# Kernel tuning notes

Measured on AMD Instinct MI355X. Metric: run time of the kernel, lower is better.

## Reference

```python
import jax, jax.numpy as jnp
import numpy as np

N = 100000
E = 1600000
D = 128
NUM_LAYERS = 3
NUM_QUANT = 3   # residual quantizer stages
K = 16          # codebook_size
COMMIT_W = 0.25


def setup_inputs() -> dict:
    key = jax.random.key(0)
    ks = jax.random.split(key, 6)
    x = jax.random.normal(ks[0], (N, D), dtype=jnp.float32)
    w_in = jax.random.normal(ks[1], (D, D), dtype=jnp.float32) / np.sqrt(D)
    b_in = jax.random.normal(ks[2], (D,), dtype=jnp.float32) * 0.01
    codebooks = jax.random.normal(ks[3], (NUM_LAYERS, NUM_QUANT, K, D), dtype=jnp.float32)
    edge_row = jax.random.randint(ks[4], (E,), 0, N, dtype=jnp.int32)
    edge_col = jax.random.randint(ks[5], (E,), 0, N, dtype=jnp.int32)
    return {"x": x, "w_in": w_in, "b_in": b_in, "codebooks": codebooks,
            "edge_row": edge_row, "edge_col": edge_col}


def _l2norm(v, eps=1e-12):
    return v / (jnp.linalg.norm(v, axis=-1, keepdims=True) + eps)


def _puregcn_conv(x, edge_row, edge_col):
    # norm = rsqrt(1 + deg); x = norm*x; x = spmm_add(adj, x) + x; x = norm*x
    n = x.shape[0]
    deg = jax.ops.segment_sum(jnp.ones_like(edge_row, dtype=x.dtype), edge_row, num_segments=n)
    norm = jax.lax.rsqrt(1.0 + deg)[:, None]
    h = norm * x
    agg = jax.ops.segment_sum(h[edge_col], edge_row, num_segments=n)  # [N, D]
    return norm * (agg + h)


def _residual_vq(x, cbs):
    # cbs: [NUM_QUANT, K, D]; cosine-sim lookup, EMA codebook (no grad to codebook)
    residual = x
    ids = []
    loss = jnp.float32(0.0)
    for q in range(NUM_QUANT):
        cb = _l2norm(cbs[q])                      # [K, D]
        sim = _l2norm(residual) @ cb.T            # [N, K]
        idx = jnp.argmax(sim, axis=-1)            # [N]
        qv = jax.lax.stop_gradient(cb[idx])       # [N, D]
        loss = loss + COMMIT_W * jnp.mean((residual - qv) ** 2)
        residual = residual - qv
        ids.append(idx.astype(jnp.int32))
    return jnp.stack(ids, axis=1), loss           # [N, NUM_QUANT], scalar


def reference(x, w_in, b_in, codebooks, edge_row, edge_col):
    # xemb: Linear (pure conv path); dropouts identity in eval
    h = x @ w_in + b_in
    id_list = []
    total_commit_loss = jnp.float32(0.0)
    for i in range(NUM_LAYERS):
        x1 = _puregcn_conv(h, edge_row, edge_col)   # lins[i] is Identity/Dropout(eval)
        ids, closs = _residual_vq(x1, codebooks[i])
        id_list.append(ids)
        total_commit_loss = total_commit_loss + closs
        h = x1 + h  # res=True, same width
    id_concat = jnp.concatenate(id_list, axis=1)    # [N, NUM_LAYERS*NUM_QUANT]
    return h, total_commit_loss, id_concat
```

## Files before the change

kernel.cpp:

```cpp
#include <hip/hip_runtime.h>

#define NN 100000
#define EE 1600000
#define DD 128
#define NL 3
#define NQ 3
#define KK 16
#define ROWS_PER_FBLOCK 64
#define FUSED_BLOCKS ((NN + ROWS_PER_FBLOCK - 1) / ROWS_PER_FBLOCK)
#define LPART_COUNT (NL * FUSED_BLOCKS)
#define EPT 8
#define EPB (256 * EPT)
#define MAXDEG 64

#define ISTRIDE 260
#define QSTRIDE (8 * ISTRIDE)
#define LAYER_CBN (NQ * QSTRIDE)
#define RSTRIDE 36
#define RBUF 144

static constexpr size_t OFF_AGG   = 0;
static constexpr size_t OFF_CSRF  = 0;
static constexpr size_t OFF_CURP  = 25600000;
static constexpr size_t OFF_CSR   = 51200000;
static constexpr size_t OFF_CBN   = 57600000;
static constexpr size_t OFF_NORM  = 57904128;
static constexpr size_t OFF_RS    = 59104128;
static constexpr size_t OFF_BSUM  = 59504640;
static constexpr size_t OFF_LPART = 59505152;
static constexpr size_t WS_NEEDED = 59805152;

__global__ __launch_bounds__(256) void k_fill_fixed(const int* __restrict__ erow,
                                                    const int* __restrict__ ecol,
                                                    int* __restrict__ cursorp,
                                                    int* __restrict__ csrf) {
    int base = blockIdx.x * EPB + threadIdx.x;
    int r[EPT], c[EPT], p[EPT];
#pragma unroll
    for (int u = 0; u < EPT; ++u) {
        int e = base + u * 256;
        r[u] = (e < EE) ? erow[e] : -1;
        c[u] = (e < EE) ? ecol[e] : 0;
    }
#pragma unroll
    for (int u = 0; u < EPT; ++u)
        if (r[u] >= 0) p[u] = atomicAdd(&cursorp[r[u] << 4], 1);
#pragma unroll
    for (int u = 0; u < EPT; ++u)
        if (r[u] >= 0 && p[u] < MAXDEG) csrf[r[u] * MAXDEG + p[u]] = c[u];
}

__global__ __launch_bounds__(1024) void k_scan1(const int* __restrict__ cursorp,
                                                int* __restrict__ rs,
                                                int* __restrict__ bsum) {
    __shared__ int s[1024];
    int tid = threadIdx.x;
    int idx = blockIdx.x * 1024 + tid;
    int v = (idx < NN) ? cursorp[idx << 4] : 0;
    s[tid] = v;
    __syncthreads();
    for (int o = 1; o < 1024; o <<= 1) {
        int t2 = s[tid];
        if (tid >= o) t2 += s[tid - o];
        __syncthreads();
        s[tid] = t2;
        __syncthreads();
    }
    if (idx < NN) rs[idx] = s[tid] - v;
    if (tid == 1023) bsum[blockIdx.x] = s[1023];
}

__global__ __launch_bounds__(128) void k_scan2(int* __restrict__ bsum, int nb) {
    __shared__ int s[128];
    int tid = threadIdx.x;
    int v = (tid < nb) ? bsum[tid] : 0;
    s[tid] = v;
    __syncthreads();
    for (int o = 1; o < 128; o <<= 1) {
        int t2 = s[tid];
        if (tid >= o) t2 += s[tid - o];
        __syncthreads();
        s[tid] = t2;
        __syncthreads();
    }
    if (tid < nb) bsum[tid] = s[tid] - v;
}

__global__ __launch_bounds__(1024) void k_scan3(const int* __restrict__ cursorp,
                                                int* __restrict__ rs,
                                                const int* __restrict__ bsum,
                                                float* __restrict__ normf) {
    int idx = blockIdx.x * 1024 + threadIdx.x;
    if (idx < NN) {
        rs[idx] += bsum[blockIdx.x];
        normf[idx] = rsqrtf(1.0f + (float)cursorp[idx << 4]);
    }
    if (idx == 0) rs[NN] = EE;
}

__global__ __launch_bounds__(256) void k_sortcompact(const int* __restrict__ cursorp,
                                                     const int* __restrict__ rs,
                                                     const int* __restrict__ csrf,
                                                     int* __restrict__ csr) {
    int wid = (blockIdx.x * 256 + threadIdx.x) >> 6;
    int l = threadIdx.x & 63;
    if (wid >= NN) return;
    int deg = cursorp[wid << 4];
    if (deg > MAXDEG) deg = MAXDEG;
    if (deg <= 0) return;
    int v = (l < deg) ? csrf[wid * MAXDEG + l] : 0x7fffffff;
    int rank = 0;
#pragma unroll 8
    for (int m = 0; m < 64; ++m) {
        int vm = __shfl(v, m);
        bool less = (vm < v) || (vm == v && m < l);
        rank += (m < deg && less) ? 1 : 0;
    }
    if (l < deg) csr[rs[wid] + rank] = v;
}

__global__ __launch_bounds__(128) void k_cbnorm(const float* __restrict__ cb,
                                                float* __restrict__ cbn) {
    __shared__ float s[128];
    int row = blockIdx.x;
    int tid = threadIdx.x;
    float v = cb[row * DD + tid];
    s[tid] = v * v;
    __syncthreads();
    for (int o = 64; o > 0; o >>= 1) {
        if (tid < o) s[tid] += s[tid + o];
        __syncthreads();
    }
    float inv = 1.0f / (sqrtf(s[0]) + 1e-12f);
    int lq = row >> 4;
    int k  = row & 15;
    int sq = tid >> 5, ii = (tid >> 2) & 7, d = tid & 3;
    cbn[(size_t)lq * QSTRIDE + ii * ISTRIDE + k * 16 + sq * 4 + d] = v * inv;
}

__global__ __launch_bounds__(256) void k_gemm(const float* __restrict__ x,
                                              const float* __restrict__ w,
                                              const float* __restrict__ bias,
                                              float* __restrict__ h) {
    __shared__ float wls[64][DD];
    __shared__ float xs[32][DD];
    int tid = threadIdx.x;
    int rbase = blockIdx.x * 32;
    int cg = tid & 31;
    int rg = tid >> 5;

#pragma unroll
    for (int p = 0; p < 4; ++p) {
        int i = p * 256 + tid;
        int r = i >> 5, c = (i & 31) * 4;
        *(float4*)&xs[r][c] = *(const float4*)&x[(size_t)(rbase + r) * DD + c];
    }

    float4 acc[4];
#pragma unroll
    for (int i = 0; i < 4; ++i) acc[i] = make_float4(0.f, 0.f, 0.f, 0.f);

    for (int chunk = 0; chunk < 2; ++chunk) {
        __syncthreads();
#pragma unroll
        for (int p = 0; p < 8; ++p) {
            int i = p * 256 + tid;
            int kr = i >> 5, c = (i & 31) * 4;
            *(float4*)&wls[kr][c] = *(const float4*)&w[(size_t)(chunk * 64 + kr) * DD + c];
        }
        __syncthreads();
#pragma unroll 4
        for (int kk = 0; kk < 64; ++kk) {
            float4 wv = *(const float4*)&wls[kk][cg * 4];
            int k = chunk * 64 + kk;
#pragma unroll
            for (int i = 0; i < 4; ++i) {
                float xv = xs[rg * 4 + i][k];
                acc[i].x += xv * wv.x; acc[i].y += xv * wv.y;
                acc[i].z += xv * wv.z; acc[i].w += xv * wv.w;
            }
        }
    }

    float4 bv = *(const float4*)&bias[cg * 4];
#pragma unroll
    for (int i = 0; i < 4; ++i) {
        float4 o;
        o.x = acc[i].x + bv.x; o.y = acc[i].y + bv.y;
        o.z = acc[i].z + bv.z; o.w = acc[i].w + bv.w;
        *(float4*)&h[(size_t)(rbase + rg * 4 + i) * DD + cg * 4] = o;
    }
}

__global__ __launch_bounds__(256) void k_spmm(const float* __restrict__ h,
                                              const float* __restrict__ normf,
                                              const int* __restrict__ rs,
                                              const int* __restrict__ csr,
                                              float* __restrict__ agg) {
    int lane = threadIdx.x & 31;
    int slot = threadIdx.x >> 5;
    int r = blockIdx.x * 8 + slot;
    int s0 = rs[r], e0 = rs[r + 1];
    int off = lane << 2;

    float ax = 0.f, ay = 0.f, az = 0.f, aw = 0.f;
    int j = s0;
    for (; j + 16 <= e0; j += 16) {
        int c[16]; float n[16]; float4 v[16];
#pragma unroll
        for (int u = 0; u < 16; ++u) c[u] = csr[j + u];
#pragma unroll
        for (int u = 0; u < 16; ++u) n[u] = normf[c[u]];
#pragma unroll
        for (int u = 0; u < 16; ++u) v[u] = *(const float4*)&h[(size_t)c[u] * DD + off];
#pragma unroll
        for (int u = 0; u < 16; ++u) {
            ax += n[u] * v[u].x; ay += n[u] * v[u].y;
            az += n[u] * v[u].z; aw += n[u] * v[u].w;
        }
    }
    for (; j + 8 <= e0; j += 8) {
        int c[8]; float n[8]; float4 v[8];
#pragma unroll
        for (int u = 0; u < 8; ++u) c[u] = csr[j + u];
#pragma unroll
        for (int u = 0; u < 8; ++u) n[u] = normf[c[u]];
#pragma unroll
        for (int u = 0; u < 8; ++u) v[u] = *(const float4*)&h[(size_t)c[u] * DD + off];
#pragma unroll
        for (int u = 0; u < 8; ++u) {
            ax += n[u] * v[u].x; ay += n[u] * v[u].y;
            az += n[u] * v[u].z; aw += n[u] * v[u].w;
        }
    }
    for (; j + 4 <= e0; j += 4) {
        int c[4]; float n[4]; float4 v[4];
#pragma unroll
        for (int u = 0; u < 4; ++u) c[u] = csr[j + u];
#pragma unroll
        for (int u = 0; u < 4; ++u) n[u] = normf[c[u]];
#pragma unroll
        for (int u = 0; u < 4; ++u) v[u] = *(const float4*)&h[(size_t)c[u] * DD + off];
#pragma unroll
        for (int u = 0; u < 4; ++u) {
            ax += n[u] * v[u].x; ay += n[u] * v[u].y;
            az += n[u] * v[u].z; aw += n[u] * v[u].w;
        }
    }
    for (; j < e0; ++j) {
        int c = csr[j];
        float ns = normf[c];
        float4 v = *(const float4*)&h[(size_t)c * DD + off];
        ax += ns * v.x;
        ay += ns * v.y;
        az += ns * v.z;
        aw += ns * v.w;
    }
    float4 o = {ax, ay, az, aw};
    *(float4*)&agg[(size_t)r * DD + off] = o;
}

__global__ __launch_bounds__(512) void k_fused(const float* __restrict__ agg,
                                               float* __restrict__ h,
                                               const float* __restrict__ normf,
                                               const float* __restrict__ cbn_layer,
                                               float* __restrict__ idsf,
                                               float* __restrict__ lpart,
                                               int layer) {
    __shared__ float cb_s[LAYER_CBN];
    __shared__ float resid_s[8][RBUF];
    __shared__ float wsum[8];
    int tid = threadIdx.x;

    {
        const float4* src = (const float4*)cbn_layer;
        float4* dst = (float4*)cb_s;
        for (int t = tid; t < LAYER_CBN / 4; t += 512) dst[t] = src[t];
    }
    __syncthreads();

    int w = tid >> 6;
    int l = tid & 63;
    int rwrd = (l >> 4) * RSTRIDE + ((2 * l) & 31);
    int sq = l & 3;
    int cb2 = ((l >> 1) & 7) * ISTRIDE + (l >> 4) * 4 + 2 * (l & 1);
    float lsum = 0.f;

    for (int it = 0; it < ROWS_PER_FBLOCK / 8; ++it) {
        int r = blockIdx.x * ROWS_PER_FBLOCK + it * 8 + w;
        if (r < NN) {
            float nr = normf[r];
            float2 hv = *(const float2*)&h[(size_t)r * DD + 2 * l];
            float2 av = *(const float2*)&agg[(size_t)r * DD + 2 * l];
            float x0 = nr * (av.x + nr * hv.x);
            float x1 = nr * (av.y + nr * hv.y);
            float r0 = x0, r1 = x1;

            for (int q = 0; q < NQ; ++q) {
                *(float2*)&resid_s[w][rwrd] = make_float2(r0, r1);

                const float* cbq = &cb_s[q * QSTRIDE];
                const float* rsd = resid_s[w];
                float pd = 0.f;
#pragma unroll
                for (int i = 0; i < 8; ++i) {
                    float4 cv = *(const float4*)&cbq[i * ISTRIDE + l * 4];
                    float4 rv = *(const float4*)&rsd[sq * RSTRIDE + i * 4];
                    pd += cv.x * rv.x + cv.y * rv.y + cv.z * rv.z + cv.w * rv.w;
                }
                pd += __shfl_xor(pd, 1);
                pd += __shfl_xor(pd, 2);

                float best = pd;
                int bk = l >> 2;
                for (int m = 4; m < 64; m <<= 1) {
                    float ov = __shfl_xor(best, m);
                    int oi = __shfl_xor(bk, m);
                    if (ov > best || (ov == best && oi < bk)) { best = ov; bk = oi; }
                }

                float2 cv2 = *(const float2*)&cb_s[q * QSTRIDE + bk * 16 + cb2];
                r0 -= cv2.x;
                r1 -= cv2.y;
                lsum += r0 * r0 + r1 * r1;

                if (l == 0) idsf[(size_t)r * (NL * NQ) + layer * NQ + q] = (float)bk;
            }

            *(float2*)&h[(size_t)r * DD + 2 * l] = make_float2(x0 + hv.x, x1 + hv.y);
        }
    }

#pragma unroll
    for (int m = 1; m < 64; m <<= 1) lsum += __shfl_xor(lsum, m);
    if (l == 0) wsum[w] = lsum;
    __syncthreads();
    if (tid == 0) {
        float tot = 0.f;
#pragma unroll
        for (int i = 0; i < 8; ++i) tot += wsum[i];
        lpart[layer * FUSED_BLOCKS + blockIdx.x] = tot * (0.25f / (float)(NN * DD));
    }
}

__global__ __launch_bounds__(256) void k_loss_reduce(const float* __restrict__ part,
                                                     float* __restrict__ out_loss) {
    __shared__ float s[256];
    float a = 0.f;
    for (int i = threadIdx.x; i < LPART_COUNT; i += 256) a += part[i];
    s[threadIdx.x] = a;
    __syncthreads();
    for (int o = 128; o > 0; o >>= 1) {
        if (threadIdx.x < o) s[threadIdx.x] += s[threadIdx.x + o];
        __syncthreads();
    }
    if (threadIdx.x == 0) out_loss[0] = s[0];
}

extern "C" void kernel_launch(void* const* d_in, const int* in_sizes, int n_in,
                              void* d_out, int out_size, void* d_ws, size_t ws_size,
                              hipStream_t stream) {
    if (ws_size < WS_NEEDED) return;

    const float* x    = (const float*)d_in[0];
    const float* w_in = (const float*)d_in[1];
    const float* b_in = (const float*)d_in[2];
    const float* cbs  = (const float*)d_in[3];
    const int*   erow = (const int*)d_in[4];
    const int*   ecol = (const int*)d_in[5];

    float* out  = (float*)d_out;
    float* hbuf = out;
    float* loss = out + (size_t)NN * DD;
    float* idsf = out + (size_t)NN * DD + 1;

    char* ws = (char*)d_ws;
    float* agg     = (float*)(ws + OFF_AGG);
    int*   csrf    = (int*)(ws + OFF_CSRF);
    int*   cursorp = (int*)(ws + OFF_CURP);
    int*   csr     = (int*)(ws + OFF_CSR);
    float* cbn     = (float*)(ws + OFF_CBN);
    float* normf   = (float*)(ws + OFF_NORM);
    int*   rs      = (int*)(ws + OFF_RS);
    int*   bsum    = (int*)(ws + OFF_BSUM);
    float* lpart   = (float*)(ws + OFF_LPART);

    hipMemsetAsync(ws + OFF_CURP, 0, 6400000, stream);

    const int NB_B  = (EE + EPB - 1) / EPB;
    const int NB_SC = (NN + 1023) / 1024;
    const int NB_W  = (NN + 3) / 4;

    k_fill_fixed<<<NB_B, 256, 0, stream>>>(erow, ecol, cursorp, csrf);
    k_scan1<<<NB_SC, 1024, 0, stream>>>(cursorp, rs, bsum);
    k_scan2<<<1, 128, 0, stream>>>(bsum, NB_SC);
    k_scan3<<<NB_SC, 1024, 0, stream>>>(cursorp, rs, bsum, normf);
    k_sortcompact<<<NB_W, 256, 0, stream>>>(cursorp, rs, csrf, csr);

    k_cbnorm<<<NL * NQ * KK, 128, 0, stream>>>(cbs, cbn);
    k_gemm<<<NN / 32, 256, 0, stream>>>(x, w_in, b_in, hbuf);

    for (int layer = 0; layer < NL; ++layer) {
        k_spmm<<<NN / 8, 256, 0, stream>>>(hbuf, normf, rs, csr, agg);
        k_fused<<<FUSED_BLOCKS, 512, 0, stream>>>(agg, hbuf, normf,
                                                  cbn + (size_t)layer * LAYER_CBN,
                                                  idsf, lpart, layer);
    }

    k_loss_reduce<<<1, 256, 0, stream>>>(lpart, loss);
}
```

Measured before the change: 852.2 us.

## Fuse SpMM gather into per-layer VQ kernel with ping-pong h buffers

Removes the separate SpMM kernel and its agg buffer by doing the neighbor gather-aggregate inside the fused VQ kernel, one 64-lane wave per row using float2 per lane. Layers ping-pong between a workspace buffer and the output so reads of the previous layer's h are not clobbered. This avoids writing and re-reading a 51 MB aggregate per layer. In exchange, the gather runs in the 512-thread block with a large codebook shared-memory footprint, so occupancy and latency hiding for the gather may be lower, and each lane issues narrower loads.

```diff
diff --git a/kernel.cpp b/kernel.cpp
--- a/kernel.cpp
+++ b/kernel.cpp
@@ -19,7 +19,7 @@
 #define RSTRIDE 36
 #define RBUF 144
 
-static constexpr size_t OFF_AGG   = 0;
+static constexpr size_t OFF_HA    = 0;
 static constexpr size_t OFF_CSRF  = 0;
 static constexpr size_t OFF_CURP  = 25600000;
 static constexpr size_t OFF_CSR   = 51200000;
@@ -192,77 +192,11 @@
     }
 }
 
-__global__ __launch_bounds__(256) void k_spmm(const float* __restrict__ h,
-                                              const float* __restrict__ normf,
-                                              const int* __restrict__ rs,
-                                              const int* __restrict__ csr,
-                                              float* __restrict__ agg) {
-    int lane = threadIdx.x & 31;
-    int slot = threadIdx.x >> 5;
-    int r = blockIdx.x * 8 + slot;
-    int s0 = rs[r], e0 = rs[r + 1];
-    int off = lane << 2;
-
-    float ax = 0.f, ay = 0.f, az = 0.f, aw = 0.f;
-    int j = s0;
-    for (; j + 16 <= e0; j += 16) {
-        int c[16]; float n[16]; float4 v[16];
-#pragma unroll
-        for (int u = 0; u < 16; ++u) c[u] = csr[j + u];
-#pragma unroll
-        for (int u = 0; u < 16; ++u) n[u] = normf[c[u]];
-#pragma unroll
-        for (int u = 0; u < 16; ++u) v[u] = *(const float4*)&h[(size_t)c[u] * DD + off];
-#pragma unroll
-        for (int u = 0; u < 16; ++u) {
-            ax += n[u] * v[u].x; ay += n[u] * v[u].y;
-            az += n[u] * v[u].z; aw += n[u] * v[u].w;
-        }
-    }
-    for (; j + 8 <= e0; j += 8) {
-        int c[8]; float n[8]; float4 v[8];
-#pragma unroll
-        for (int u = 0; u < 8; ++u) c[u] = csr[j + u];
-#pragma unroll
-        for (int u = 0; u < 8; ++u) n[u] = normf[c[u]];
-#pragma unroll
-        for (int u = 0; u < 8; ++u) v[u] = *(const float4*)&h[(size_t)c[u] * DD + off];
-#pragma unroll
-        for (int u = 0; u < 8; ++u) {
-            ax += n[u] * v[u].x; ay += n[u] * v[u].y;
-            az += n[u] * v[u].z; aw += n[u] * v[u].w;
-        }
-    }
-    for (; j + 4 <= e0; j += 4) {
-        int c[4]; float n[4]; float4 v[4];
-#pragma unroll
-        for (int u = 0; u < 4; ++u) c[u] = csr[j + u];
-#pragma unroll
-        for (int u = 0; u < 4; ++u) n[u] = normf[c[u]];
-#pragma unroll
-        for (int u = 0; u < 4; ++u) v[u] = *(const float4*)&h[(size_t)c[u] * DD + off];
-#pragma unroll
-        for (int u = 0; u < 4; ++u) {
-            ax += n[u] * v[u].x; ay += n[u] * v[u].y;
-            az += n[u] * v[u].z; aw += n[u] * v[u].w;
-        }
-    }
-    for (; j < e0; ++j) {
-        int c = csr[j];
-        float ns = normf[c];
-        float4 v = *(const float4*)&h[(size_t)c * DD + off];
-        ax += ns * v.x;
-        ay += ns * v.y;
-        az += ns * v.z;
-        aw += ns * v.w;
-    }
-    float4 o = {ax, ay, az, aw};
-    *(float4*)&agg[(size_t)r * DD + off] = o;
-}
-
-__global__ __launch_bounds__(512) void k_fused(const float* __restrict__ agg,
-                                               float* __restrict__ h,
+__global__ __launch_bounds__(512) void k_layer(const float* __restrict__ hin,
+                                               float* __restrict__ hout,
                                                const float* __restrict__ normf,
+                                               const int* __restrict__ rs,
+                                               const int* __restrict__ csr,
                                                const float* __restrict__ cbn_layer,
                                                float* __restrict__ idsf,
                                                float* __restrict__ lpart,
@@ -281,6 +215,7 @@
 
     int w = tid >> 6;
     int l = tid & 63;
+    int off = 2 * l;
     int rwrd = (l >> 4) * RSTRIDE + ((2 * l) & 31);
     int sq = l & 3;
     int cb2 = ((l >> 1) & 7) * ISTRIDE + (l >> 4) * 4 + 2 * (l & 1);
@@ -289,11 +224,44 @@
     for (int it = 0; it < ROWS_PER_FBLOCK / 8; ++it) {
         int r = blockIdx.x * ROWS_PER_FBLOCK + it * 8 + w;
         if (r < NN) {
+            int s0 = rs[r], e0 = rs[r + 1];
+
+            float a0 = 0.f, a1 = 0.f;
+            int j = s0;
+            for (; j + 8 <= e0; j += 8) {
+                int c[8]; float n[8]; float2 v[8];
+#pragma unroll
+                for (int u = 0; u < 8; ++u) c[u] = csr[j + u];
+#pragma unroll
+                for (int u = 0; u < 8; ++u) n[u] = normf[c[u]];
+#pragma unroll
+                for (int u = 0; u < 8; ++u) v[u] = *(const float2*)&hin[(size_t)c[u] * DD + off];
+#pragma unroll
+                for (int u = 0; u < 8; ++u) { a0 += n[u] * v[u].x; a1 += n[u] * v[u].y; }
+            }
+            for (; j + 4 <= e0; j += 4) {
+                int c[4]; float n[4]; float2 v[4];
+#pragma unroll
+                for (int u = 0; u < 4; ++u) c[u] = csr[j + u];
+#pragma unroll
+                for (int u = 0; u < 4; ++u) n[u] = normf[c[u]];
+#pragma unroll
+                for (int u = 0; u < 4; ++u) v[u] = *(const float2*)&hin[(size_t)c[u] * DD + off];
+#pragma unroll
+                for (int u = 0; u < 4; ++u) { a0 += n[u] * v[u].x; a1 += n[u] * v[u].y; }
+            }
+            for (; j < e0; ++j) {
+                int c = csr[j];
+                float ns = normf[c];
+                float2 v = *(const float2*)&hin[(size_t)c * DD + off];
+                a0 += ns * v.x;
+                a1 += ns * v.y;
+            }
+
             float nr = normf[r];
-            float2 hv = *(const float2*)&h[(size_t)r * DD + 2 * l];
-            float2 av = *(const float2*)&agg[(size_t)r * DD + 2 * l];
-            float x0 = nr * (av.x + nr * hv.x);
-            float x1 = nr * (av.y + nr * hv.y);
+            float2 hv = *(const float2*)&hin[(size_t)r * DD + off];
+            float x0 = nr * (a0 + nr * hv.x);
+            float x1 = nr * (a1 + nr * hv.y);
             float r0 = x0, r1 = x1;
 
             for (int q = 0; q < NQ; ++q) {
@@ -327,7 +295,7 @@
                 if (l == 0) idsf[(size_t)r * (NL * NQ) + layer * NQ + q] = (float)bk;
             }
 
-            *(float2*)&h[(size_t)r * DD + 2 * l] = make_float2(x0 + hv.x, x1 + hv.y);
+            *(float2*)&hout[(size_t)r * DD + off] = make_float2(x0 + hv.x, x1 + hv.y);
         }
     }
 
@@ -370,12 +338,12 @@
     const int*   ecol = (const int*)d_in[5];
 
     float* out  = (float*)d_out;
-    float* hbuf = out;
+    float* hout = out;
     float* loss = out + (size_t)NN * DD;
     float* idsf = out + (size_t)NN * DD + 1;
 
     char* ws = (char*)d_ws;
-    float* agg     = (float*)(ws + OFF_AGG);
+    float* ha      = (float*)(ws + OFF_HA);
     int*   csrf    = (int*)(ws + OFF_CSRF);
     int*   cursorp = (int*)(ws + OFF_CURP);
     int*   csr     = (int*)(ws + OFF_CSR);
@@ -398,14 +366,18 @@
     k_sortcompact<<<NB_W, 256, 0, stream>>>(cursorp, rs, csrf, csr);
 
     k_cbnorm<<<NL * NQ * KK, 128, 0, stream>>>(cbs, cbn);
-    k_gemm<<<NN / 32, 256, 0, stream>>>(x, w_in, b_in, hbuf);
-
-    for (int layer = 0; layer < NL; ++layer) {
-        k_spmm<<<NN / 8, 256, 0, stream>>>(hbuf, normf, rs, csr, agg);
-        k_fused<<<FUSED_BLOCKS, 512, 0, stream>>>(agg, hbuf, normf,
-                                                  cbn + (size_t)layer * LAYER_CBN,
-                                                  idsf, lpart, layer);
-    }
+
+    k_gemm<<<NN / 32, 256, 0, stream>>>(x, w_in, b_in, ha);
+
+    k_layer<<<FUSED_BLOCKS, 512, 0, stream>>>(ha, hout, normf, rs, csr,
+                                              cbn + (size_t)0 * LAYER_CBN,
+                                              idsf, lpart, 0);
+    k_layer<<<FUSED_BLOCKS, 512, 0, stream>>>(hout, ha, normf, rs, csr,
+                                              cbn + (size_t)1 * LAYER_CBN,
+                                              idsf, lpart, 1);
+    k_layer<<<FUSED_BLOCKS, 512, 0, stream>>>(ha, hout, normf, rs, csr,
+                                              cbn + (size_t)2 * LAYER_CBN,
+                                              idsf, lpart, 2);
 
     k_loss_reduce<<<1, 256, 0, stream>>>(lpart, loss);
 }
```

Measured after the change: 817.3 us (median of 2 runs). 1.04x faster.

## Fuse SpMM gather into per-layer VQ kernel with ping-pong h buffers

Applied to the files above, without the earlier changes.

Merges the separate SpMM and fused-VQ kernels into a single per-layer kernel. The neighbour aggregation is computed into shared memory and consumed immediately, so the agg array no longer makes a round trip through global memory. Two h buffers are used in ping-pong fashion to avoid read/write hazards, and the layer loop is unrolled so the final result lands in the output buffer. The trade-offs are lower parallelism for the gather (fewer, larger 512-thread blocks with more shared memory) and lost latency hiding between the gather and VQ phases.

```diff
diff --git a/kernel.cpp b/kernel.cpp
--- a/kernel.cpp
+++ b/kernel.cpp
@@ -19,7 +19,7 @@
 #define RSTRIDE 36
 #define RBUF 144
 
-static constexpr size_t OFF_AGG   = 0;
+static constexpr size_t OFF_HA    = 0;
 static constexpr size_t OFF_CSRF  = 0;
 static constexpr size_t OFF_CURP  = 25600000;
 static constexpr size_t OFF_CSR   = 51200000;
@@ -192,82 +192,17 @@
     }
 }
 
-__global__ __launch_bounds__(256) void k_spmm(const float* __restrict__ h,
-                                              const float* __restrict__ normf,
-                                              const int* __restrict__ rs,
-                                              const int* __restrict__ csr,
-                                              float* __restrict__ agg) {
-    int lane = threadIdx.x & 31;
-    int slot = threadIdx.x >> 5;
-    int r = blockIdx.x * 8 + slot;
-    int s0 = rs[r], e0 = rs[r + 1];
-    int off = lane << 2;
-
-    float ax = 0.f, ay = 0.f, az = 0.f, aw = 0.f;
-    int j = s0;
-    for (; j + 16 <= e0; j += 16) {
-        int c[16]; float n[16]; float4 v[16];
-#pragma unroll
-        for (int u = 0; u < 16; ++u) c[u] = csr[j + u];
-#pragma unroll
-        for (int u = 0; u < 16; ++u) n[u] = normf[c[u]];
-#pragma unroll
-        for (int u = 0; u < 16; ++u) v[u] = *(const float4*)&h[(size_t)c[u] * DD + off];
-#pragma unroll
-        for (int u = 0; u < 16; ++u) {
-            ax += n[u] * v[u].x; ay += n[u] * v[u].y;
-            az += n[u] * v[u].z; aw += n[u] * v[u].w;
-        }
-    }
-    for (; j + 8 <= e0; j += 8) {
-        int c[8]; float n[8]; float4 v[8];
-#pragma unroll
-        for (int u = 0; u < 8; ++u) c[u] = csr[j + u];
-#pragma unroll
-        for (int u = 0; u < 8; ++u) n[u] = normf[c[u]];
-#pragma unroll
-        for (int u = 0; u < 8; ++u) v[u] = *(const float4*)&h[(size_t)c[u] * DD + off];
-#pragma unroll
-        for (int u = 0; u < 8; ++u) {
-            ax += n[u] * v[u].x; ay += n[u] * v[u].y;
-            az += n[u] * v[u].z; aw += n[u] * v[u].w;
-        }
-    }
-    for (; j + 4 <= e0; j += 4) {
-        int c[4]; float n[4]; float4 v[4];
-#pragma unroll
-        for (int u = 0; u < 4; ++u) c[u] = csr[j + u];
-#pragma unroll
-        for (int u = 0; u < 4; ++u) n[u] = normf[c[u]];
-#pragma unroll
-        for (int u = 0; u < 4; ++u) v[u] = *(const float4*)&h[(size_t)c[u] * DD + off];
-#pragma unroll
-        for (int u = 0; u < 4; ++u) {
-            ax += n[u] * v[u].x; ay += n[u] * v[u].y;
-            az += n[u] * v[u].z; aw += n[u] * v[u].w;
-        }
-    }
-    for (; j < e0; ++j) {
-        int c = csr[j];
-        float ns = normf[c];
-        float4 v = *(const float4*)&h[(size_t)c * DD + off];
-        ax += ns * v.x;
-        ay += ns * v.y;
-        az += ns * v.z;
-        aw += ns * v.w;
-    }
-    float4 o = {ax, ay, az, aw};
-    *(float4*)&agg[(size_t)r * DD + off] = o;
-}
-
-__global__ __launch_bounds__(512) void k_fused(const float* __restrict__ agg,
-                                               float* __restrict__ h,
+__global__ __launch_bounds__(512) void k_layer(const float* __restrict__ hin,
+                                               float* __restrict__ hout,
                                                const float* __restrict__ normf,
+                                               const int* __restrict__ rs,
+                                               const int* __restrict__ csr,
                                                const float* __restrict__ cbn_layer,
                                                float* __restrict__ idsf,
                                                float* __restrict__ lpart,
                                                int layer) {
     __shared__ float cb_s[LAYER_CBN];
+    __shared__ float agg_s[8][2][DD];
     __shared__ float resid_s[8][RBUF];
     __shared__ float wsum[8];
     int tid = threadIdx.x;
@@ -281,53 +216,118 @@
 
     int w = tid >> 6;
     int l = tid & 63;
+    int half = l >> 5;
+    int off4 = (l & 31) << 2;
     int rwrd = (l >> 4) * RSTRIDE + ((2 * l) & 31);
     int sq = l & 3;
     int cb2 = ((l >> 1) & 7) * ISTRIDE + (l >> 4) * 4 + 2 * (l & 1);
     float lsum = 0.f;
-
-    for (int it = 0; it < ROWS_PER_FBLOCK / 8; ++it) {
-        int r = blockIdx.x * ROWS_PER_FBLOCK + it * 8 + w;
-        if (r < NN) {
-            float nr = normf[r];
-            float2 hv = *(const float2*)&h[(size_t)r * DD + 2 * l];
-            float2 av = *(const float2*)&agg[(size_t)r * DD + 2 * l];
-            float x0 = nr * (av.x + nr * hv.x);
-            float x1 = nr * (av.y + nr * hv.y);
-            float r0 = x0, r1 = x1;
-
-            for (int q = 0; q < NQ; ++q) {
-                *(float2*)&resid_s[w][rwrd] = make_float2(r0, r1);
-
-                const float* cbq = &cb_s[q * QSTRIDE];
-                const float* rsd = resid_s[w];
-                float pd = 0.f;
-#pragma unroll
-                for (int i = 0; i < 8; ++i) {
-                    float4 cv = *(const float4*)&cbq[i * ISTRIDE + l * 4];
-                    float4 rv = *(const float4*)&rsd[sq * RSTRIDE + i * 4];
-                    pd += cv.x * rv.x + cv.y * rv.y + cv.z * rv.z + cv.w * rv.w;
+    int base = blockIdx.x * ROWS_PER_FBLOCK + w;
+
+    for (int p = 0; p < 4; ++p) {
+        int rA = base + p * 16;
+        int row = rA + half * 8;
+
+        int s0 = 0, e0 = 0;
+        if (row < NN) { s0 = rs[row]; e0 = rs[row + 1]; }
+        float ax = 0.f, ay = 0.f, az = 0.f, aw = 0.f;
+        int j = s0;
+        for (; j + 16 <= e0; j += 16) {
+            int c[16]; float n[16]; float4 v[16];
+#pragma unroll
+            for (int u = 0; u < 16; ++u) c[u] = csr[j + u];
+#pragma unroll
+            for (int u = 0; u < 16; ++u) n[u] = normf[c[u]];
+#pragma unroll
+            for (int u = 0; u < 16; ++u) v[u] = *(const float4*)&hin[(size_t)c[u] * DD + off4];
+#pragma unroll
+            for (int u = 0; u < 16; ++u) {
+                ax += n[u] * v[u].x; ay += n[u] * v[u].y;
+                az += n[u] * v[u].z; aw += n[u] * v[u].w;
+            }
+        }
+        for (; j + 8 <= e0; j += 8) {
+            int c[8]; float n[8]; float4 v[8];
+#pragma unroll
+            for (int u = 0; u < 8; ++u) c[u] = csr[j + u];
+#pragma unroll
+            for (int u = 0; u < 8; ++u) n[u] = normf[c[u]];
+#pragma unroll
+            for (int u = 0; u < 8; ++u) v[u] = *(const float4*)&hin[(size_t)c[u] * DD + off4];
+#pragma unroll
+            for (int u = 0; u < 8; ++u) {
+                ax += n[u] * v[u].x; ay += n[u] * v[u].y;
+                az += n[u] * v[u].z; aw += n[u] * v[u].w;
+            }
+        }
+        for (; j + 4 <= e0; j += 4) {
+            int c[4]; float n[4]; float4 v[4];
+#pragma unroll
+            for (int u = 0; u < 4; ++u) c[u] = csr[j + u];
+#pragma unroll
+            for (int u = 0; u < 4; ++u) n[u] = normf[c[u]];
+#pragma unroll
+            for (int u = 0; u < 4; ++u) v[u] = *(const float4*)&hin[(size_t)c[u] * DD + off4];
+#pragma unroll
+            for (int u = 0; u < 4; ++u) {
+                ax += n[u] * v[u].x; ay += n[u] * v[u].y;
+                az += n[u] * v[u].z; aw += n[u] * v[u].w;
+            }
+        }
+        for (; j < e0; ++j) {
+            int c = csr[j];
+            float ns = normf[c];
+            float4 v = *(const float4*)&hin[(size_t)c * DD + off4];
+            ax += ns * v.x;
+            ay += ns * v.y;
+            az += ns * v.z;
+            aw += ns * v.w;
+        }
+        *(float4*)&agg_s[w][half][off4] = make_float4(ax, ay, az, aw);
+
+#pragma unroll
+        for (int xr = 0; xr < 2; ++xr) {
+            int r = rA + xr * 8;
+            if (r < NN) {
+                float nr = normf[r];
+                float2 hv = *(const float2*)&hin[(size_t)r * DD + 2 * l];
+                float2 av = *(const float2*)&agg_s[w][xr][2 * l];
+                float x0 = nr * (av.x + nr * hv.x);
+                float x1 = nr * (av.y + nr * hv.y);
+                *(float2*)&hout[(size_t)r * DD + 2 * l] = make_float2(x0 + hv.x, x1 + hv.y);
+                float r0 = x0, r1 = x1;
+
+                for (int q = 0; q < NQ; ++q) {
+                    *(float2*)&resid_s[w][rwrd] = make_float2(r0, r1);
+
+                    const float* cbq = &cb_s[q * QSTRIDE];
+                    const float* rsd = resid_s[w];
+                    float pd = 0.f;
+#pragma unroll
+                    for (int i = 0; i < 8; ++i) {
+                        float4 cv = *(const float4*)&cbq[i * ISTRIDE + l * 4];
+                        float4 rv = *(const float4*)&rsd[sq * RSTRIDE + i * 4];
+                        pd += cv.x * rv.x + cv.y * rv.y + cv.z * rv.z + cv.w * rv.w;
+                    }
+                    pd += __shfl_xor(pd, 1);
+                    pd += __shfl_xor(pd, 2);
+
+                    float best = pd;
+                    int bk = l >> 2;
+                    for (int m = 4; m < 64; m <<= 1) {
+                        float ov = __shfl_xor(best, m);
+                        int oi = __shfl_xor(bk, m);
+                        if (ov > best || (ov == best && oi < bk)) { best = ov; bk = oi; }
+                    }
+
+                    float2 cv2 = *(const float2*)&cb_s[q * QSTRIDE + bk * 16 + cb2];
+                    r0 -= cv2.x;
+                    r1 -= cv2.y;
+                    lsum += r0 * r0 + r1 * r1;
+
+                    if (l == 0) idsf[(size_t)r * (NL * NQ) + layer * NQ + q] = (float)bk;
                 }
-                pd += __shfl_xor(pd, 1);
-                pd += __shfl_xor(pd, 2);
-
-                float best = pd;
-                int bk = l >> 2;
-                for (int m = 4; m < 64; m <<= 1) {
-                    float ov = __shfl_xor(best, m);
-                    int oi = __shfl_xor(bk, m);
-                    if (ov > best || (ov == best && oi < bk)) { best = ov; bk = oi; }
-                }
-
-                float2 cv2 = *(const float2*)&cb_s[q * QSTRIDE + bk * 16 + cb2];
-                r0 -= cv2.x;
-                r1 -= cv2.y;
-                lsum += r0 * r0 + r1 * r1;
-
-                if (l == 0) idsf[(size_t)r * (NL * NQ) + layer * NQ + q] = (float)bk;
             }
-
-            *(float2*)&h[(size_t)r * DD + 2 * l] = make_float2(x0 + hv.x, x1 + hv.y);
         }
     }
 
@@ -370,12 +370,12 @@
     const int*   ecol = (const int*)d_in[5];
 
     float* out  = (float*)d_out;
-    float* hbuf = out;
+    float* hout = out;
     float* loss = out + (size_t)NN * DD;
     float* idsf = out + (size_t)NN * DD + 1;
 
     char* ws = (char*)d_ws;
-    float* agg     = (float*)(ws + OFF_AGG);
+    float* ha      = (float*)(ws + OFF_HA);
     int*   csrf    = (int*)(ws + OFF_CSRF);
     int*   cursorp = (int*)(ws + OFF_CURP);
     int*   csr     = (int*)(ws + OFF_CSR);
@@ -398,14 +398,18 @@
     k_sortcompact<<<NB_W, 256, 0, stream>>>(cursorp, rs, csrf, csr);
 
     k_cbnorm<<<NL * NQ * KK, 128, 0, stream>>>(cbs, cbn);
-    k_gemm<<<NN / 32, 256, 0, stream>>>(x, w_in, b_in, hbuf);
-
-    for (int layer = 0; layer < NL; ++layer) {
-        k_spmm<<<NN / 8, 256, 0, stream>>>(hbuf, normf, rs, csr, agg);
-        k_fused<<<FUSED_BLOCKS, 512, 0, stream>>>(agg, hbuf, normf,
-                                                  cbn + (size_t)layer * LAYER_CBN,
-                                                  idsf, lpart, layer);
-    }
+
+    k_gemm<<<NN / 32, 256, 0, stream>>>(x, w_in, b_in, ha);
+
+    k_layer<<<FUSED_BLOCKS, 512, 0, stream>>>(ha, hout, normf, rs, csr,
+                                              cbn + (size_t)0 * LAYER_CBN,
+                                              idsf, lpart, 0);
+    k_layer<<<FUSED_BLOCKS, 512, 0, stream>>>(hout, ha, normf, rs, csr,
+                                              cbn + (size_t)1 * LAYER_CBN,
+                                              idsf, lpart, 1);
+    k_layer<<<FUSED_BLOCKS, 512, 0, stream>>>(ha, hout, normf, rs, csr,
+                                              cbn + (size_t)2 * LAYER_CBN,
+                                              idsf, lpart, 2);
 
     k_loss_reduce<<<1, 256, 0, stream>>>(lpart, loss);
 }
```

Result: slower. 1.048 ms (+23.0%).
